# Performance work log

Measured on AMD Instinct MI355X. Metric: run time of the kernel, lower is better.

Reference implementation:

```python
import jax, jax.numpy as jnp
import numpy as np

N = 100000      # nodes
E = 1600000     # edges (before self-loops)
IN = 128        # in_channels
HID = 32        # hidden_channels
H = 4           # heads of conv1
OUT = 40        # out_channels (classes)
NEG_SLOPE = 0.2 # PyG GATConv default


def _gat_layer(x, edge_index, W, att_src, att_dst, bias, heads, ch, concat):
    """PyG-style GATConv (add_self_loops=True, eval mode so no dropout).
    x: [n, d_in]; W: [d_in, heads*ch]; att_src/att_dst: [heads, ch]; bias: [heads*ch] or [ch]."""
    n = x.shape[0]
    loops = jnp.arange(n, dtype=edge_index.dtype)
    src = jnp.concatenate([edge_index[0], loops])   # [E+n] message sources (x_j)
    dst = jnp.concatenate([edge_index[1], loops])   # [E+n] message targets (x_i)

    h = (x @ W).reshape(n, heads, ch)               # [n, H, C]
    a_s = jnp.sum(h * att_src, axis=-1)             # [n, H] -> alpha_j component
    a_d = jnp.sum(h * att_dst, axis=-1)             # [n, H] -> alpha_i component

    e = jax.nn.leaky_relu(a_s[src] + a_d[dst], NEG_SLOPE)      # [E+n, H]
    # segment softmax over destination node
    m = jax.ops.segment_max(e, dst, num_segments=n)            # [n, H]
    p = jnp.exp(e - m[dst])
    s = jax.ops.segment_sum(p, dst, num_segments=n)            # [n, H]
    alpha = p / (s[dst] + 1e-16)                                # [E+n, H]

    out = jax.ops.segment_sum(h[src] * alpha[:, :, None], dst, num_segments=n)  # [n, H, C]
    out = out.reshape(n, heads * ch) if concat else out.mean(axis=1)
    return out + bias


def setup_inputs() -> dict:
    key = jax.random.key(0)
    ks = jax.random.split(key, 10)
    sc1 = 1.0 / np.sqrt(IN)
    sc2 = 1.0 / np.sqrt(H * HID)
    return {
        "x": jax.random.normal(ks[0], (N, IN), dtype=jnp.float32),
        "edge_index": jax.random.randint(ks[1], (2, E), 0, N, dtype=jnp.int64),
        "W1": jax.random.normal(ks[2], (IN, H * HID), dtype=jnp.float32) * sc1,
        "a_src1": jax.random.normal(ks[3], (H, HID), dtype=jnp.float32) * sc1,
        "a_dst1": jax.random.normal(ks[4], (H, HID), dtype=jnp.float32) * sc1,
        "b1": jnp.zeros((H * HID,), dtype=jnp.float32),
        "W2": jax.random.normal(ks[5], (H * HID, OUT), dtype=jnp.float32) * sc2,
        "a_src2": jax.random.normal(ks[6], (1, OUT), dtype=jnp.float32) * sc2,
        "a_dst2": jax.random.normal(ks[7], (1, OUT), dtype=jnp.float32) * sc2,
        "b2": jnp.zeros((OUT,), dtype=jnp.float32),
    }


def reference(x, edge_index, W1, a_src1, a_dst1, b1, W2, a_src2, a_dst2, b2):
    h = _gat_layer(x, edge_index, W1, a_src1, a_dst1, b1, heads=H, ch=HID, concat=True)
    h = jax.nn.elu(h)
    # dropout is identity in eval mode
    h = _gat_layer(h, edge_index, W2, a_src2, a_dst2, b2, heads=1, ch=OUT, concat=False)
    return jax.nn.log_softmax(h, axis=1)
```

## Files before the change

kernel.cpp:

```cpp
#include <hip/hip_runtime.h>

#define N_NODES 100000
#define N_EDGES 1600000
#define N_ETOT  1700000
#define NB_BUCK   391
#define PART_BLOCKS 512
#define PART_CHUNK  3328

typedef unsigned int uint32;
typedef __attribute__((ext_vector_type(8))) short bf16x8;
typedef __attribute__((ext_vector_type(4))) float f32x4;

__device__ __forceinline__ unsigned short f2bf(float f) {
  uint32 u = __float_as_uint(f);
  u += 0x7FFFu + ((u >> 16) & 1u);
  return (unsigned short)(u >> 16);
}
__device__ __forceinline__ float bf_lo(uint32 w) { return __uint_as_float(w << 16); }
__device__ __forceinline__ float bf_hi(uint32 w) { return __uint_as_float(w & 0xFFFF0000u); }


__global__ __launch_bounds__(256) void k_bcount(const int* __restrict__ ei,
                                                int* __restrict__ bcnt) {
  __shared__ int hist[NB_BUCK];
  const int t = threadIdx.x;
  for (int b = t; b < NB_BUCK; b += 256) hist[b] = 0;
  __syncthreads();
  const int c0 = blockIdx.x * PART_CHUNK;
  const int c1 = (c0 + PART_CHUNK < N_ETOT) ? c0 + PART_CHUNK : N_ETOT;
  for (int i = c0 + t; i < c1; i += 256) {
    int dst = (i < N_EDGES) ? ei[N_EDGES + i] : (i - N_EDGES);
    atomicAdd(&hist[dst >> 8], 1);
  }
  __syncthreads();
  for (int b = t; b < NB_BUCK; b += 256)
    if (hist[b]) atomicAdd(&bcnt[b], hist[b]);
}

__global__ void k_bscan(const int* __restrict__ bcnt, int* __restrict__ pbase,
                        int* __restrict__ bcur, int* __restrict__ rs) {
  __shared__ int sm[512];
  int t = threadIdx.x;
  int v = (t < NB_BUCK) ? bcnt[t] : 0;
  sm[t] = v;
  __syncthreads();
  for (int off = 1; off < 512; off <<= 1) {
    int xv = (t >= off) ? sm[t - off] : 0;
    __syncthreads();
    sm[t] += xv;
    __syncthreads();
  }
  if (t < NB_BUCK) { int e = sm[t] - v; pbase[t] = e; bcur[t] = e; }
  if (t == 0) { pbase[NB_BUCK] = N_ETOT; rs[N_NODES] = N_ETOT; }
}

__global__ __launch_bounds__(256) void k_part(const int* __restrict__ ei,
                                              int* __restrict__ bcur,
                                              uint2* __restrict__ pairs) {
  __shared__ int hist[NB_BUCK];
  __shared__ int base[NB_BUCK];
  const int t = threadIdx.x;
  for (int b = t; b < NB_BUCK; b += 256) hist[b] = 0;
  __syncthreads();
  const int c0 = blockIdx.x * PART_CHUNK;
  const int c1 = (c0 + PART_CHUNK < N_ETOT) ? c0 + PART_CHUNK : N_ETOT;
  for (int i = c0 + t; i < c1; i += 256) {
    int dst = (i < N_EDGES) ? ei[N_EDGES + i] : (i - N_EDGES);
    atomicAdd(&hist[dst >> 8], 1);
  }
  __syncthreads();
  for (int b = t; b < NB_BUCK; b += 256) {
    int h = hist[b];
    base[b] = h ? atomicAdd(&bcur[b], h) : 0;
    hist[b] = 0;
  }
  __syncthreads();
  for (int i = c0 + t; i < c1; i += 256) {
    int src, dst;
    if (i < N_EDGES) { src = ei[i]; dst = ei[N_EDGES + i]; }
    else             { src = i - N_EDGES; dst = src; }
    int b = dst >> 8;
    int r = atomicAdd(&hist[b], 1);
    pairs[base[b] + r] = make_uint2((uint32)src, (uint32)dst);
  }
}

__global__ __launch_bounds__(256) void k_scatter2f(const int* __restrict__ pbase,
                                                   const uint2* __restrict__ pairs,
                                                   int* __restrict__ rs,
                                                   int* __restrict__ csr) {
  __shared__ int cnt[256];
  __shared__ int scn[256];
  __shared__ int cur[256];
  const int t = threadIdx.x;
  const int lo = blockIdx.x << 8;
  cnt[t] = 0;
  __syncthreads();
  const int p0 = pbase[blockIdx.x], p1 = pbase[blockIdx.x + 1];
  for (int i = p0 + t; i < p1; i += 256) atomicAdd(&cnt[pairs[i].y & 255], 1);
  __syncthreads();
  int v = cnt[t];
  scn[t] = v;
  __syncthreads();
  for (int off = 1; off < 256; off <<= 1) {
    int xv = (t >= off) ? scn[t - off] : 0;
    __syncthreads();
    scn[t] += xv;
    __syncthreads();
  }
  int e = p0 + scn[t] - v;
  cur[t] = e;
  if (lo + t < N_NODES) rs[lo + t] = e;
  __syncthreads();
  for (int i = p0 + t; i < p1; i += 256) {
    uint2 pr = pairs[i];
    int pos = atomicAdd(&cur[pr.y & 255], 1);
    csr[pos] = (int)pr.x;
  }
}


__global__ void k_prep(const float* __restrict__ W1, const float* __restrict__ W2,
                       unsigned short* __restrict__ W1t, unsigned short* __restrict__ W2t) {
  int i = blockIdx.x * 256 + threadIdx.x;
  if (i < 128 * 128) {
    int c = i >> 7, k = i & 127;
    W1t[i] = f2bf(W1[k * 128 + c]);
  }
  int j = i - 128 * 128;
  if (j >= 0 && j < 48 * 128) {
    int c = j >> 7, k = j & 127;
    W2t[j] = (c < 40) ? f2bf(W2[k * 40 + c]) : (unsigned short)0;
  }
}


__global__ __launch_bounds__(256) void k_gemm1m(const float* __restrict__ x,
                                                const unsigned short* __restrict__ W1t,
                                                unsigned short* __restrict__ h1b) {
  __shared__ unsigned short As[128 * 128];
  const int t = threadIdx.x;
  const int rbase = blockIdx.x * 128;
  const float4* x4 = (const float4*)x;
  #pragma unroll
  for (int it = 0; it < 8; ++it) {
    int idx = it * 256 + t;
    int r = idx >> 4, c = idx & 15;
    int gr = rbase + r;
    float4 f0 = make_float4(0.f, 0.f, 0.f, 0.f), f1 = f0;
    if (gr < N_NODES) { f0 = x4[(size_t)gr * 32 + c * 2]; f1 = x4[(size_t)gr * 32 + c * 2 + 1]; }
    ushort4 u0, u1;
    u0.x = f2bf(f0.x); u0.y = f2bf(f0.y); u0.z = f2bf(f0.z); u0.w = f2bf(f0.w);
    u1.x = f2bf(f1.x); u1.y = f2bf(f1.y); u1.z = f2bf(f1.z); u1.w = f2bf(f1.w);
    int sc = c ^ (r & 7);
    *(ushort4*)&As[r * 128 + sc * 8] = u0;
    *(ushort4*)&As[r * 128 + sc * 8 + 4] = u1;
  }
  __syncthreads();

  const int wid = t >> 6, lane = t & 63;
  const int wm = wid >> 1, wn = wid & 1;
  const int m0 = wm * 64, n0 = wn * 64;
  const int lr = lane & 15, lk = lane >> 4;

  bf16x8 b[4][4];
  #pragma unroll
  for (int kk = 0; kk < 4; ++kk)
    #pragma unroll
    for (int nt = 0; nt < 4; ++nt) {
      int col = n0 + nt * 16 + lr;
      b[kk][nt] = *(const bf16x8*)&W1t[col * 128 + kk * 32 + lk * 8];
    }

  f32x4 acc[4][4];
  #pragma unroll
  for (int mt = 0; mt < 4; ++mt)
    #pragma unroll
    for (int nt = 0; nt < 4; ++nt) acc[mt][nt] = (f32x4)(0.f);

  #pragma unroll
  for (int mt = 0; mt < 4; ++mt) {
    int row = m0 + mt * 16 + lr;
    #pragma unroll
    for (int kk = 0; kk < 4; ++kk) {
      int c = kk * 4 + lk;
      int sc = c ^ (row & 7);
      bf16x8 a = *(const bf16x8*)&As[row * 128 + sc * 8];
      #pragma unroll
      for (int nt = 0; nt < 4; ++nt)
        acc[mt][nt] = __builtin_amdgcn_mfma_f32_16x16x32_bf16(a, b[kk][nt], acc[mt][nt], 0, 0, 0);
    }
  }

  #pragma unroll
  for (int mt = 0; mt < 4; ++mt)
    #pragma unroll
    for (int nt = 0; nt < 4; ++nt) {
      int col = n0 + nt * 16 + lr;
      #pragma unroll
      for (int r = 0; r < 4; ++r) {
        int gr = rbase + m0 + mt * 16 + lk * 4 + r;
        if (gr < N_NODES) h1b[(size_t)gr * 128 + col] = f2bf(acc[mt][nt][r]);
      }
    }
}

__global__ __launch_bounds__(256) void k_gemm2m(const unsigned short* __restrict__ xab,
                                                const unsigned short* __restrict__ W2t,
                                                unsigned short* __restrict__ h2b) {
  __shared__ unsigned short As[128 * 128];
  const int t = threadIdx.x;
  const int rbase = blockIdx.x * 128;
  #pragma unroll
  for (int it = 0; it < 8; ++it) {
    int idx = it * 256 + t;
    int r = idx >> 4, c = idx & 15;
    int gr = rbase + r;
    uint4 v = make_uint4(0u, 0u, 0u, 0u);
    if (gr < N_NODES) v = *(const uint4*)&xab[(size_t)gr * 128 + c * 8];
    int sc = c ^ (r & 7);
    *(uint4*)&As[r * 128 + sc * 8] = v;
  }
  __syncthreads();

  const int wid = t >> 6, lane = t & 63;
  const int m0 = wid * 32;
  const int lr = lane & 15, lk = lane >> 4;

  bf16x8 b[4][3];
  #pragma unroll
  for (int kk = 0; kk < 4; ++kk)
    #pragma unroll
    for (int nt = 0; nt < 3; ++nt) {
      int col = nt * 16 + lr;
      b[kk][nt] = *(const bf16x8*)&W2t[col * 128 + kk * 32 + lk * 8];
    }

  f32x4 acc[2][3];
  #pragma unroll
  for (int mt = 0; mt < 2; ++mt)
    #pragma unroll
    for (int nt = 0; nt < 3; ++nt) acc[mt][nt] = (f32x4)(0.f);

  #pragma unroll
  for (int mt = 0; mt < 2; ++mt) {
    int row = m0 + mt * 16 + lr;
    #pragma unroll
    for (int kk = 0; kk < 4; ++kk) {
      int c = kk * 4 + lk;
      int sc = c ^ (row & 7);
      bf16x8 a = *(const bf16x8*)&As[row * 128 + sc * 8];
      #pragma unroll
      for (int nt = 0; nt < 3; ++nt)
        acc[mt][nt] = __builtin_amdgcn_mfma_f32_16x16x32_bf16(a, b[kk][nt], acc[mt][nt], 0, 0, 0);
    }
  }

  #pragma unroll
  for (int mt = 0; mt < 2; ++mt)
    #pragma unroll
    for (int nt = 0; nt < 3; ++nt) {
      int col = nt * 16 + lr;
      if (col < 40) {
        #pragma unroll
        for (int r = 0; r < 4; ++r) {
          int gr = rbase + m0 + mt * 16 + lk * 4 + r;
          if (gr < N_NODES) h2b[(size_t)gr * 64 + col] = f2bf(acc[mt][nt][r]);
        }
      }
    }
}


__global__ void k_scores1(const unsigned short* __restrict__ h1b,
                          const float* __restrict__ a_src,
                          const float* __restrict__ a_dst,
                          float* __restrict__ so, float* __restrict__ dvo) {
  int n = blockIdx.x * 256 + threadIdx.x;
  if (n >= N_NODES) return;
  const uint4* hr = (const uint4*)(h1b + (size_t)n * 128);
  const float4* As = (const float4*)a_src;
  const float4* Ad = (const float4*)a_dst;
  float sa[4] = {0.f,0.f,0.f,0.f}, da[4] = {0.f,0.f,0.f,0.f};
  #pragma unroll
  for (int q = 0; q < 16; ++q) {
    int hh = q >> 2;
    uint4 v = hr[q];
    float f0 = bf_lo(v.x), f1 = bf_hi(v.x), f2 = bf_lo(v.y), f3 = bf_hi(v.y);
    float f4 = bf_lo(v.z), f5 = bf_hi(v.z), f6 = bf_lo(v.w), f7 = bf_hi(v.w);
    float4 A0 = As[q * 2], A1 = As[q * 2 + 1];
    float4 D0 = Ad[q * 2], D1 = Ad[q * 2 + 1];
    sa[hh] += f0*A0.x + f1*A0.y + f2*A0.z + f3*A0.w + f4*A1.x + f5*A1.y + f6*A1.z + f7*A1.w;
    da[hh] += f0*D0.x + f1*D0.y + f2*D0.z + f3*D0.w + f4*D1.x + f5*D1.y + f6*D1.z + f7*D1.w;
  }
  #pragma unroll
  for (int hh = 0; hh < 4; ++hh) { so[n * 4 + hh] = sa[hh]; dvo[n * 4 + hh] = da[hh]; }
}

__global__ void k_scores2(unsigned short* __restrict__ h2b,
                          const float* __restrict__ a_src,
                          const float* __restrict__ a_dst,
                          float* __restrict__ dvo) {
  int n = blockIdx.x * 256 + threadIdx.x;
  if (n >= N_NODES) return;
  const uint4* hr = (const uint4*)(h2b + (size_t)n * 64);
  float sa = 0.f, da = 0.f;
  #pragma unroll
  for (int q = 0; q < 5; ++q) {
    uint4 v = hr[q];
    float f0 = bf_lo(v.x), f1 = bf_hi(v.x), f2 = bf_lo(v.y), f3 = bf_hi(v.y);
    float f4 = bf_lo(v.z), f5 = bf_hi(v.z), f6 = bf_lo(v.w), f7 = bf_hi(v.w);
    const float* A = a_src + q * 8;
    const float* D = a_dst + q * 8;
    sa += f0*A[0] + f1*A[1] + f2*A[2] + f3*A[3] + f4*A[4] + f5*A[5] + f6*A[6] + f7*A[7];
    da += f0*D[0] + f1*D[1] + f2*D[2] + f3*D[3] + f4*D[4] + f5*D[5] + f6*D[6] + f7*D[7];
  }
  *(float*)((char*)h2b + (size_t)n * 128 + 80) = sa;
  dvo[n] = da;
}


#define ACC8(A, off, u, p) \
  A[(off)+0] += (p)*bf_lo(u.x); A[(off)+1] += (p)*bf_hi(u.x); \
  A[(off)+2] += (p)*bf_lo(u.y); A[(off)+3] += (p)*bf_hi(u.y); \
  A[(off)+4] += (p)*bf_lo(u.z); A[(off)+5] += (p)*bf_hi(u.z); \
  A[(off)+6] += (p)*bf_lo(u.w); A[(off)+7] += (p)*bf_hi(u.w);

__global__ __launch_bounds__(256) void k_gather1(const int* __restrict__ rs,
                                                 const int* __restrict__ csr,
                                                 const unsigned short* __restrict__ h1b,
                                                 const float* __restrict__ asrc,
                                                 const float* __restrict__ adst,
                                                 const float* __restrict__ bias,
                                                 unsigned short* __restrict__ xab) {
  int gid = blockIdx.x * 256 + threadIdx.x;
  int n = gid >> 3;
  if (n >= N_NODES) return;
  int lane = gid & 7;
  int hh = lane >> 1;
  float adn = adst[n * 4 + hh];
  int beg = rs[n], end = rs[n + 1];
  float s = 0.f;
  float A[16];
  #pragma unroll
  for (int j = 0; j < 16; ++j) A[j] = 0.f;
  const uint4* hp = (const uint4*)h1b;
  const size_t lb = (size_t)lane * 2;
  int i = beg;
  for (; i + 2 <= end; i += 2) {
    int s0 = csr[i], s1 = csr[i + 1];
    float w0 = asrc[s0 * 4 + hh];
    float w1 = asrc[s1 * 4 + hh];
    uint4 x0 = hp[(size_t)s0 * 16 + lb];
    uint4 x1 = hp[(size_t)s0 * 16 + lb + 1];
    uint4 y0 = hp[(size_t)s1 * 16 + lb];
    uint4 y1 = hp[(size_t)s1 * 16 + lb + 1];
    float v0 = w0 + adn; v0 = (v0 > 0.f) ? v0 : 0.2f * v0;
    float v1 = w1 + adn; v1 = (v1 > 0.f) ? v1 : 0.2f * v1;
    float p0 = __expf(v0), p1 = __expf(v1);
    s += p0 + p1;
    ACC8(A, 0, x0, p0); ACC8(A, 8, x1, p0);
    ACC8(A, 0, y0, p1); ACC8(A, 8, y1, p1);
  }
  if (i < end) {
    int s0 = csr[i];
    float v0 = asrc[s0 * 4 + hh] + adn; v0 = (v0 > 0.f) ? v0 : 0.2f * v0;
    uint4 x0 = hp[(size_t)s0 * 16 + lb];
    uint4 x1 = hp[(size_t)s0 * 16 + lb + 1];
    float p0 = __expf(v0);
    s += p0;
    ACC8(A, 0, x0, p0); ACC8(A, 8, x1, p0);
  }
  float inv = 1.f / (s + 1e-16f);
  int c = lane * 16;
  unsigned short us[16];
  #pragma unroll
  for (int j = 0; j < 16; ++j) {
    float ov = A[j] * inv + bias[c + j];
    ov = (ov > 0.f) ? ov : __expf(ov) - 1.f;
    us[j] = f2bf(ov);
  }
  uint4 w0, w1;
  w0.x = (uint32)us[0] | ((uint32)us[1] << 16);
  w0.y = (uint32)us[2] | ((uint32)us[3] << 16);
  w0.z = (uint32)us[4] | ((uint32)us[5] << 16);
  w0.w = (uint32)us[6] | ((uint32)us[7] << 16);
  w1.x = (uint32)us[8] | ((uint32)us[9] << 16);
  w1.y = (uint32)us[10] | ((uint32)us[11] << 16);
  w1.z = (uint32)us[12] | ((uint32)us[13] << 16);
  w1.w = (uint32)us[14] | ((uint32)us[15] << 16);
  *(uint4*)&xab[(size_t)n * 128 + c] = w0;
  *(uint4*)&xab[(size_t)n * 128 + c + 8] = w1;
}

__global__ __launch_bounds__(256) void k_gather2(const int* __restrict__ rs,
                                                 const int* __restrict__ csr,
                                                 const unsigned short* __restrict__ h2b,
                                                 const float* __restrict__ adst,
                                                 float* __restrict__ agg) {
  int gid = blockIdx.x * 256 + threadIdx.x;
  int n = gid >> 3;
  if (n >= N_NODES) return;
  int lane = gid & 7;
  float adn = adst[n];
  int beg = rs[n], end = rs[n + 1];
  float s = 0.f;
  float c0 = 0.f, c1 = 0.f, c2 = 0.f, c3 = 0.f, c4 = 0.f;
  const char* hb = (const char*)h2b;
  int i = beg;
  for (; i + 2 <= end; i += 2) {
    int s0 = csr[i], s1 = csr[i + 1];
    const char* r0 = hb + (size_t)s0 * 128;
    const char* r1 = hb + (size_t)s1 * 128;
    float w0 = *(const float*)(r0 + 80);
    float w1 = *(const float*)(r1 + 80);
    uint2 a0 = *(const uint2*)(r0 + lane * 8);
    uint2 a1 = *(const uint2*)(r1 + lane * 8);
    unsigned short e0 = *(const unsigned short*)(r0 + 64 + lane * 2);
    unsigned short e1 = *(const unsigned short*)(r1 + 64 + lane * 2);
    float v0 = w0 + adn; v0 = (v0 > 0.f) ? v0 : 0.2f * v0;
    float v1 = w1 + adn; v1 = (v1 > 0.f) ? v1 : 0.2f * v1;
    float p0 = __expf(v0), p1 = __expf(v1);
    s += p0 + p1;
    c0 += p0 * bf_lo(a0.x) + p1 * bf_lo(a1.x);
    c1 += p0 * bf_hi(a0.x) + p1 * bf_hi(a1.x);
    c2 += p0 * bf_lo(a0.y) + p1 * bf_lo(a1.y);
    c3 += p0 * bf_hi(a0.y) + p1 * bf_hi(a1.y);
    c4 += p0 * __uint_as_float(((uint32)e0) << 16) + p1 * __uint_as_float(((uint32)e1) << 16);
  }
  if (i < end) {
    int s0 = csr[i];
    const char* r0 = hb + (size_t)s0 * 128;
    float v0 = *(const float*)(r0 + 80) + adn; v0 = (v0 > 0.f) ? v0 : 0.2f * v0;
    uint2 a0 = *(const uint2*)(r0 + lane * 8);
    unsigned short e0 = *(const unsigned short*)(r0 + 64 + lane * 2);
    float p0 = __expf(v0);
    s += p0;
    c0 += p0 * bf_lo(a0.x); c1 += p0 * bf_hi(a0.x);
    c2 += p0 * bf_lo(a0.y); c3 += p0 * bf_hi(a0.y);
    c4 += p0 * __uint_as_float(((uint32)e0) << 16);
  }
  float inv = 1.f / (s + 1e-16f);
  float4 w = make_float4(c0 * inv, c1 * inv, c2 * inv, c3 * inv);
  *(float4*)&agg[(size_t)n * 40 + lane * 4] = w;
  agg[(size_t)n * 40 + 32 + lane] = c4 * inv;
}


__global__ void k_finish(const float* __restrict__ agg, const float* __restrict__ bias,
                         float* __restrict__ out) {
  int n = blockIdx.x * 256 + threadIdx.x;
  if (n >= N_NODES) return;
  float v[40];
  float mx = -3.0e38f;
  #pragma unroll
  for (int c = 0; c < 40; ++c) { v[c] = agg[n * 40 + c] + bias[c]; mx = fmaxf(mx, v[c]); }
  float sum = 0.f;
  #pragma unroll
  for (int c = 0; c < 40; ++c) sum += __expf(v[c] - mx);
  float l = __logf(sum);
  #pragma unroll
  for (int c = 0; c < 40; ++c) out[n * 40 + c] = v[c] - mx - l;
}


extern "C" void kernel_launch(void* const* d_in, const int* in_sizes, int n_in,
                              void* d_out, int out_size, void* d_ws, size_t ws_size,
                              hipStream_t stream) {
  const float* x   = (const float*)d_in[0];
  const int*   ei  = (const int*)  d_in[1];
  const float* W1  = (const float*)d_in[2];
  const float* aS1 = (const float*)d_in[3];
  const float* aD1 = (const float*)d_in[4];
  const float* b1  = (const float*)d_in[5];
  const float* W2  = (const float*)d_in[6];
  const float* aS2 = (const float*)d_in[7];
  const float* aD2 = (const float*)d_in[8];
  const float* b2  = (const float*)d_in[9];
  float* out = (float*)d_out;
  (void)in_sizes; (void)n_in; (void)out_size; (void)ws_size;

  unsigned short* W1t = (unsigned short*)d_ws;
  unsigned short* W2t = W1t + 128 * 128;
  unsigned short* h1b = W2t + 48 * 128;
  unsigned short* xab = h1b + (size_t)N_NODES * 128;
  unsigned short* h2b = xab + (size_t)N_NODES * 128;
  float* agg2 = (float*)(h2b + (size_t)N_NODES * 64);
  float* s1s  = agg2 + (size_t)N_NODES * 40;
  float* s1d  = s1s + (size_t)N_NODES * 4;
  float* s2d  = s1d + (size_t)N_NODES * 4;
  int* rs    = (int*)(s2d + N_NODES);
  int* bcnt  = rs + N_NODES + 1;
  int* pbase = bcnt + NB_BUCK;
  int* bcur  = pbase + NB_BUCK + 1;
  int* csr   = bcur + NB_BUCK;
  uint2* pairs = (uint2*)(csr + N_ETOT);

  hipMemsetAsync(bcnt, 0, NB_BUCK * sizeof(int), stream);
  k_prep     <<<88, 256, 0, stream>>>(W1, W2, W1t, W2t);
  k_bcount   <<<PART_BLOCKS, 256, 0, stream>>>(ei, bcnt);
  k_bscan    <<<1, 512, 0, stream>>>(bcnt, pbase, bcur, rs);
  k_part     <<<PART_BLOCKS, 256, 0, stream>>>(ei, bcur, pairs);
  k_scatter2f<<<NB_BUCK, 256, 0, stream>>>(pbase, pairs, rs, csr);

  k_gemm1m  <<<(N_NODES + 127) / 128, 256, 0, stream>>>(x, W1t, h1b);
  k_scores1 <<<(N_NODES + 255) / 256, 256, 0, stream>>>(h1b, aS1, aD1, s1s, s1d);
  k_gather1 <<<(N_NODES * 8 + 255) / 256, 256, 0, stream>>>(rs, csr, h1b, s1s, s1d, b1, xab);

  k_gemm2m  <<<(N_NODES + 127) / 128, 256, 0, stream>>>(xab, W2t, h2b);
  k_scores2 <<<(N_NODES + 255) / 256, 256, 0, stream>>>(h2b, aS2, aD2, s2d);
  k_gather2 <<<(N_NODES * 8 + 255) / 256, 256, 0, stream>>>(rs, csr, h2b, s2d, agg2);
  k_finish  <<<(N_NODES + 255) / 256, 256, 0, stream>>>(agg2, b2, out);
}
```

Measured before the change: 247.2 us.

## Fuse attention scores into GEMM epilogues, log-softmax into gather, pack edge pairs

Computes the per-node source and destination attention scores directly from the MFMA accumulators using cross-lane shuffles. This removes the separate k_scores1 and k_scores2 kernels, which re-read h1b and h2b. The final bias plus log-softmax moves into k_gather2 using 8-lane shuffle reductions, which removes k_finish and the agg2 round trip through memory. Partition pairs are packed into one 32-bit word (17-bit src plus the low 8 bits of dst) instead of uint2, halving pair traffic at the cost of assuming node ids fit in 17 bits. Scores are now computed from fp32 accumulators rather than the bf16-rounded h, which slightly changes numerics.

```diff
diff --git a/kernel.cpp b/kernel.cpp
--- a/kernel.cpp
+++ b/kernel.cpp
@@ -56,7 +56,7 @@
 
 __global__ __launch_bounds__(256) void k_part(const int* __restrict__ ei,
                                               int* __restrict__ bcur,
-                                              uint2* __restrict__ pairs) {
+                                              uint32* __restrict__ pairs) {
   __shared__ int hist[NB_BUCK];
   __shared__ int base[NB_BUCK];
   const int t = threadIdx.x;
@@ -81,12 +81,12 @@
     else             { src = i - N_EDGES; dst = src; }
     int b = dst >> 8;
     int r = atomicAdd(&hist[b], 1);
-    pairs[base[b] + r] = make_uint2((uint32)src, (uint32)dst);
+    pairs[base[b] + r] = (uint32)src | (((uint32)dst & 255u) << 17);
   }
 }
 
 __global__ __launch_bounds__(256) void k_scatter2f(const int* __restrict__ pbase,
-                                                   const uint2* __restrict__ pairs,
+                                                   const uint32* __restrict__ pairs,
                                                    int* __restrict__ rs,
                                                    int* __restrict__ csr) {
   __shared__ int cnt[256];
@@ -97,7 +97,7 @@
   cnt[t] = 0;
   __syncthreads();
   const int p0 = pbase[blockIdx.x], p1 = pbase[blockIdx.x + 1];
-  for (int i = p0 + t; i < p1; i += 256) atomicAdd(&cnt[pairs[i].y & 255], 1);
+  for (int i = p0 + t; i < p1; i += 256) atomicAdd(&cnt[pairs[i] >> 17], 1);
   __syncthreads();
   int v = cnt[t];
   scn[t] = v;
@@ -113,9 +113,9 @@
   if (lo + t < N_NODES) rs[lo + t] = e;
   __syncthreads();
   for (int i = p0 + t; i < p1; i += 256) {
-    uint2 pr = pairs[i];
-    int pos = atomicAdd(&cur[pr.y & 255], 1);
-    csr[pos] = (int)pr.x;
+    uint32 pr = pairs[i];
+    int pos = atomicAdd(&cur[pr >> 17], 1);
+    csr[pos] = (int)(pr & 0x1FFFFu);
   }
 }
 
@@ -137,7 +137,11 @@
 
 __global__ __launch_bounds__(256) void k_gemm1m(const float* __restrict__ x,
                                                 const unsigned short* __restrict__ W1t,
-                                                unsigned short* __restrict__ h1b) {
+                                                const float* __restrict__ aS1,
+                                                const float* __restrict__ aD1,
+                                                unsigned short* __restrict__ h1b,
+                                                float* __restrict__ s1s,
+                                                float* __restrict__ s1d) {
   __shared__ unsigned short As[128 * 128];
   const int t = threadIdx.x;
   const int rbase = blockIdx.x * 128;
@@ -164,13 +168,15 @@
   const int lr = lane & 15, lk = lane >> 4;
 
   bf16x8 b[4][4];
-  #pragma unroll
-  for (int kk = 0; kk < 4; ++kk)
-    #pragma unroll
-    for (int nt = 0; nt < 4; ++nt) {
-      int col = n0 + nt * 16 + lr;
+  float as_v[4], ad_v[4];
+  #pragma unroll
+  for (int nt = 0; nt < 4; ++nt) {
+    int col = n0 + nt * 16 + lr;
+    as_v[nt] = aS1[col]; ad_v[nt] = aD1[col];
+    #pragma unroll
+    for (int kk = 0; kk < 4; ++kk)
       b[kk][nt] = *(const bf16x8*)&W1t[col * 128 + kk * 32 + lk * 8];
-    }
+  }
 
   f32x4 acc[4][4];
   #pragma unroll
@@ -203,11 +209,37 @@
         if (gr < N_NODES) h1b[(size_t)gr * 128 + col] = f2bf(acc[mt][nt][r]);
       }
     }
+
+  const int h0 = wn * 2;
+  #pragma unroll
+  for (int mt = 0; mt < 4; ++mt)
+    #pragma unroll
+    for (int r = 0; r < 4; ++r) {
+      float sa0 = acc[mt][0][r] * as_v[0] + acc[mt][1][r] * as_v[1];
+      float sa1 = acc[mt][2][r] * as_v[2] + acc[mt][3][r] * as_v[3];
+      float da0 = acc[mt][0][r] * ad_v[0] + acc[mt][1][r] * ad_v[1];
+      float da1 = acc[mt][2][r] * ad_v[2] + acc[mt][3][r] * ad_v[3];
+      #pragma unroll
+      for (int m = 1; m < 16; m <<= 1) {
+        sa0 += __shfl_xor(sa0, m); sa1 += __shfl_xor(sa1, m);
+        da0 += __shfl_xor(da0, m); da1 += __shfl_xor(da1, m);
+      }
+      if (lr == ((mt << 2) | r)) {
+        int gr = rbase + m0 + mt * 16 + lk * 4 + r;
+        if (gr < N_NODES) {
+          s1s[gr * 4 + h0] = sa0; s1s[gr * 4 + h0 + 1] = sa1;
+          s1d[gr * 4 + h0] = da0; s1d[gr * 4 + h0 + 1] = da1;
+        }
+      }
+    }
 }
 
 __global__ __launch_bounds__(256) void k_gemm2m(const unsigned short* __restrict__ xab,
                                                 const unsigned short* __restrict__ W2t,
-                                                unsigned short* __restrict__ h2b) {
+                                                const float* __restrict__ aS2,
+                                                const float* __restrict__ aD2,
+                                                unsigned short* __restrict__ h2b,
+                                                float* __restrict__ s2d) {
   __shared__ unsigned short As[128 * 128];
   const int t = threadIdx.x;
   const int rbase = blockIdx.x * 128;
@@ -228,13 +260,16 @@
   const int lr = lane & 15, lk = lane >> 4;
 
   bf16x8 b[4][3];
-  #pragma unroll
-  for (int kk = 0; kk < 4; ++kk)
-    #pragma unroll
-    for (int nt = 0; nt < 3; ++nt) {
-      int col = nt * 16 + lr;
+  float as_v[3], ad_v[3];
+  #pragma unroll
+  for (int nt = 0; nt < 3; ++nt) {
+    int col = nt * 16 + lr;
+    as_v[nt] = (col < 40) ? aS2[col] : 0.f;
+    ad_v[nt] = (col < 40) ? aD2[col] : 0.f;
+    #pragma unroll
+    for (int kk = 0; kk < 4; ++kk)
       b[kk][nt] = *(const bf16x8*)&W2t[col * 128 + kk * 32 + lk * 8];
-    }
+  }
 
   f32x4 acc[2][3];
   #pragma unroll
@@ -269,54 +304,25 @@
         }
       }
     }
-}
-
-
-__global__ void k_scores1(const unsigned short* __restrict__ h1b,
-                          const float* __restrict__ a_src,
-                          const float* __restrict__ a_dst,
-                          float* __restrict__ so, float* __restrict__ dvo) {
-  int n = blockIdx.x * 256 + threadIdx.x;
-  if (n >= N_NODES) return;
-  const uint4* hr = (const uint4*)(h1b + (size_t)n * 128);
-  const float4* As = (const float4*)a_src;
-  const float4* Ad = (const float4*)a_dst;
-  float sa[4] = {0.f,0.f,0.f,0.f}, da[4] = {0.f,0.f,0.f,0.f};
-  #pragma unroll
-  for (int q = 0; q < 16; ++q) {
-    int hh = q >> 2;
-    uint4 v = hr[q];
-    float f0 = bf_lo(v.x), f1 = bf_hi(v.x), f2 = bf_lo(v.y), f3 = bf_hi(v.y);
-    float f4 = bf_lo(v.z), f5 = bf_hi(v.z), f6 = bf_lo(v.w), f7 = bf_hi(v.w);
-    float4 A0 = As[q * 2], A1 = As[q * 2 + 1];
-    float4 D0 = Ad[q * 2], D1 = Ad[q * 2 + 1];
-    sa[hh] += f0*A0.x + f1*A0.y + f2*A0.z + f3*A0.w + f4*A1.x + f5*A1.y + f6*A1.z + f7*A1.w;
-    da[hh] += f0*D0.x + f1*D0.y + f2*D0.z + f3*D0.w + f4*D1.x + f5*D1.y + f6*D1.z + f7*D1.w;
-  }
-  #pragma unroll
-  for (int hh = 0; hh < 4; ++hh) { so[n * 4 + hh] = sa[hh]; dvo[n * 4 + hh] = da[hh]; }
-}
-
-__global__ void k_scores2(unsigned short* __restrict__ h2b,
-                          const float* __restrict__ a_src,
-                          const float* __restrict__ a_dst,
-                          float* __restrict__ dvo) {
-  int n = blockIdx.x * 256 + threadIdx.x;
-  if (n >= N_NODES) return;
-  const uint4* hr = (const uint4*)(h2b + (size_t)n * 64);
-  float sa = 0.f, da = 0.f;
-  #pragma unroll
-  for (int q = 0; q < 5; ++q) {
-    uint4 v = hr[q];
-    float f0 = bf_lo(v.x), f1 = bf_hi(v.x), f2 = bf_lo(v.y), f3 = bf_hi(v.y);
-    float f4 = bf_lo(v.z), f5 = bf_hi(v.z), f6 = bf_lo(v.w), f7 = bf_hi(v.w);
-    const float* A = a_src + q * 8;
-    const float* D = a_dst + q * 8;
-    sa += f0*A[0] + f1*A[1] + f2*A[2] + f3*A[3] + f4*A[4] + f5*A[5] + f6*A[6] + f7*A[7];
-    da += f0*D[0] + f1*D[1] + f2*D[2] + f3*D[3] + f4*D[4] + f5*D[5] + f6*D[6] + f7*D[7];
-  }
-  *(float*)((char*)h2b + (size_t)n * 128 + 80) = sa;
-  dvo[n] = da;
+
+  #pragma unroll
+  for (int mt = 0; mt < 2; ++mt)
+    #pragma unroll
+    for (int r = 0; r < 4; ++r) {
+      float sa = acc[mt][0][r] * as_v[0] + acc[mt][1][r] * as_v[1] + acc[mt][2][r] * as_v[2];
+      float da = acc[mt][0][r] * ad_v[0] + acc[mt][1][r] * ad_v[1] + acc[mt][2][r] * ad_v[2];
+      #pragma unroll
+      for (int m = 1; m < 16; m <<= 1) {
+        sa += __shfl_xor(sa, m); da += __shfl_xor(da, m);
+      }
+      if (lr == ((mt << 2) | r)) {
+        int gr = rbase + m0 + mt * 16 + lk * 4 + r;
+        if (gr < N_NODES) {
+          *(float*)((char*)h2b + (size_t)gr * 128 + 80) = sa;
+          s2d[gr] = da;
+        }
+      }
+    }
 }
 
 
@@ -397,7 +403,8 @@
                                                  const int* __restrict__ csr,
                                                  const unsigned short* __restrict__ h2b,
                                                  const float* __restrict__ adst,
-                                                 float* __restrict__ agg) {
+                                                 const float* __restrict__ bias,
+                                                 float* __restrict__ out) {
   int gid = blockIdx.x * 256 + threadIdx.x;
   int n = gid >> 3;
   if (n >= N_NODES) return;
@@ -441,26 +448,24 @@
     c4 += p0 * __uint_as_float(((uint32)e0) << 16);
   }
   float inv = 1.f / (s + 1e-16f);
-  float4 w = make_float4(c0 * inv, c1 * inv, c2 * inv, c3 * inv);
-  *(float4*)&agg[(size_t)n * 40 + lane * 4] = w;
-  agg[(size_t)n * 40 + 32 + lane] = c4 * inv;
-}
-
-
-__global__ void k_finish(const float* __restrict__ agg, const float* __restrict__ bias,
-                         float* __restrict__ out) {
-  int n = blockIdx.x * 256 + threadIdx.x;
-  if (n >= N_NODES) return;
-  float v[40];
-  float mx = -3.0e38f;
-  #pragma unroll
-  for (int c = 0; c < 40; ++c) { v[c] = agg[n * 40 + c] + bias[c]; mx = fmaxf(mx, v[c]); }
-  float sum = 0.f;
-  #pragma unroll
-  for (int c = 0; c < 40; ++c) sum += __expf(v[c] - mx);
-  float l = __logf(sum);
-  #pragma unroll
-  for (int c = 0; c < 40; ++c) out[n * 40 + c] = v[c] - mx - l;
+  float4 bv = *(const float4*)&bias[lane * 4];
+  float b4 = bias[32 + lane];
+  float v0 = c0 * inv + bv.x;
+  float v1 = c1 * inv + bv.y;
+  float v2 = c2 * inv + bv.z;
+  float v3 = c3 * inv + bv.w;
+  float v4 = c4 * inv + b4;
+  float mx = fmaxf(fmaxf(fmaxf(v0, v1), fmaxf(v2, v3)), v4);
+  #pragma unroll
+  for (int m = 1; m < 8; m <<= 1) mx = fmaxf(mx, __shfl_xor(mx, m, 8));
+  float se = __expf(v0 - mx) + __expf(v1 - mx) + __expf(v2 - mx)
+           + __expf(v3 - mx) + __expf(v4 - mx);
+  #pragma unroll
+  for (int m = 1; m < 8; m <<= 1) se += __shfl_xor(se, m, 8);
+  float l = __logf(se) + mx;
+  float4 o = make_float4(v0 - l, v1 - l, v2 - l, v3 - l);
+  *(float4*)&out[(size_t)n * 40 + lane * 4] = o;
+  out[(size_t)n * 40 + 32 + lane] = v4 - l;
 }
 
 
@@ -485,8 +490,7 @@
   unsigned short* h1b = W2t + 48 * 128;
   unsigned short* xab = h1b + (size_t)N_NODES * 128;
   unsigned short* h2b = xab + (size_t)N_NODES * 128;
-  float* agg2 = (float*)(h2b + (size_t)N_NODES * 64);
-  float* s1s  = agg2 + (size_t)N_NODES * 40;
+  float* s1s  = (float*)(h2b + (size_t)N_NODES * 64);
   float* s1d  = s1s + (size_t)N_NODES * 4;
   float* s2d  = s1d + (size_t)N_NODES * 4;
   int* rs    = (int*)(s2d + N_NODES);
@@ -494,7 +498,7 @@
   int* pbase = bcnt + NB_BUCK;
   int* bcur  = pbase + NB_BUCK + 1;
   int* csr   = bcur + NB_BUCK;
-  uint2* pairs = (uint2*)(csr + N_ETOT);
+  uint32* pairs = (uint32*)(csr + N_ETOT);
 
   hipMemsetAsync(bcnt, 0, NB_BUCK * sizeof(int), stream);
   k_prep     <<<88, 256, 0, stream>>>(W1, W2, W1t, W2t);
@@ -503,12 +507,9 @@
   k_part     <<<PART_BLOCKS, 256, 0, stream>>>(ei, bcur, pairs);
   k_scatter2f<<<NB_BUCK, 256, 0, stream>>>(pbase, pairs, rs, csr);
 
-  k_gemm1m  <<<(N_NODES + 127) / 128, 256, 0, stream>>>(x, W1t, h1b);
-  k_scores1 <<<(N_NODES + 255) / 256, 256, 0, stream>>>(h1b, aS1, aD1, s1s, s1d);
+  k_gemm1m  <<<(N_NODES + 127) / 128, 256, 0, stream>>>(x, W1t, aS1, aD1, h1b, s1s, s1d);
   k_gather1 <<<(N_NODES * 8 + 255) / 256, 256, 0, stream>>>(rs, csr, h1b, s1s, s1d, b1, xab);
 
-  k_gemm2m  <<<(N_NODES + 127) / 128, 256, 0, stream>>>(xab, W2t, h2b);
-  k_scores2 <<<(N_NODES + 255) / 256, 256, 0, stream>>>(h2b, aS2, aD2, s2d);
-  k_gather2 <<<(N_NODES * 8 + 255) / 256, 256, 0, stream>>>(rs, csr, h2b, s2d, agg2);
-  k_finish  <<<(N_NODES + 255) / 256, 256, 0, stream>>>(agg2, b2, out);
-}
+  k_gemm2m  <<<(N_NODES + 127) / 128, 256, 0, stream>>>(xab, W2t, aS2, aD2, h2b, s2d);
+  k_gather2 <<<(N_NODES * 8 + 255) / 256, 256, 0, stream>>>(rs, csr, h2b, s2d, b2, out);
+}
```

Measured after the change: 234.9 us. 5.0% less time.
